# Kernel tuning notes

Measured on AMD Instinct MI355X. Metric: run time of the kernel, lower is better.

The kernel has to match this reference:

```python
import jax, jax.numpy as jnp
import numpy as np

NUM_STEPS = 20
BETA = 0.9
THR = 1.0
B, D, H, O = 8192, 784, 128, 10


def setup_inputs() -> dict:
    key = jax.random.key(0)
    k1, k2, k3, k4, k5 = jax.random.split(key, 5)
    x = jax.random.uniform(k1, (B, D), jnp.float32)  # rates in [0,1]
    lim1 = 1.0 / np.sqrt(D)
    lim2 = 1.0 / np.sqrt(H)
    fc1_w = jax.random.uniform(k2, (H, D), jnp.float32, -lim1, lim1)
    fc1_b = jax.random.uniform(k3, (H,), jnp.float32, -lim1, lim1)
    fc2_w = jax.random.uniform(k4, (O, H), jnp.float32, -lim2, lim2)
    fc2_b = jax.random.uniform(k5, (O,), jnp.float32, -lim2, lim2)
    return {"x": x, "fc1_w": fc1_w, "fc1_b": fc1_b, "fc2_w": fc2_w, "fc2_b": fc2_b}


def heaviside(u):
    return (u > 0).astype(u.dtype)


def lif_step(mem, cur):
    # snntorch Leaky, reset_mechanism='subtract':
    #   reset computed from incoming mem, then mem = beta*mem + cur - reset*thr
    reset = heaviside(mem - THR)
    mem = BETA * mem + cur - reset * THR
    spk = heaviside(mem - THR)
    return spk, mem


def reference(x, fc1_w, fc1_b, fc2_w, fc2_b):
    batch = x.shape[0]
    # spikegen.rate: per-step Bernoulli with probability x (fixed key -> deterministic)
    skey = jax.random.key(42)
    x_spike = jax.random.bernoulli(skey, x, (NUM_STEPS, batch, x.shape[1])).astype(x.dtype)

    mem1 = jnp.zeros((batch, fc1_w.shape[0]), x.dtype)
    mem2 = jnp.zeros((batch, fc2_w.shape[0]), x.dtype)

    def step(carry, x_t):
        m1, m2 = carry
        cur1 = x_t @ fc1_w.T + fc1_b          # [B,128]
        spk1, m1 = lif_step(m1, cur1)
        cur2 = spk1 @ fc2_w.T + fc2_b         # [B,10]
        spk2, m2 = lif_step(m2, cur2)
        return (m1, m2), spk2

    _, spk2_stack = jax.lax.scan(step, (mem1, mem2), x_spike)  # [T,B,10]
    return spk2_stack.sum(axis=0) / NUM_STEPS
```

## Files before the change

### kernel.cpp

```cpp
#include <hip/hip_runtime.h>
#include <cstdint>


#define T_STEPS 20
#define B_SZ   8192
#define D_SZ   784
#define H_SZ   128
#define O_SZ   10
#define CUR1_BYTES  83886080u
#define MASKS_OFF   83886080u
#define WP_OFF      84541440u
#define THR_OFF     101539840u

typedef __attribute__((ext_vector_type(8))) short short8;
typedef __attribute__((ext_vector_type(4))) float f32x4;
typedef unsigned short ushort_t;

#define ROTL_ASM(dst, src, sh)                                        \
  asm("v_alignbit_b32 %0, %1, %1, %2" : "=v"(dst) : "v"(src), "n"(32 - (sh)))

__device__ __forceinline__ void threefry_0_42(uint32_t c1,
                                              uint32_t& o0, uint32_t& o1) {
  const uint32_t ks1 = 42u;
  const uint32_t ks2 = 42u ^ 0x1BD11BDAu;
  uint32_t x0, x1, r;
  x1 = c1 + ks1;
  x0 = x1;
  ROTL_ASM(r, x1, 13); x1 = r ^ x0;
#define TF_R(rot) { x0 += x1; ROTL_ASM(r, x1, rot); x1 = r ^ x0; }
#define TF_IR(C1, K0, rot) { x1 += (C1); x0 = x0 + (K0) + x1; \
                             ROTL_ASM(r, x1, rot); x1 = r ^ x0; }
  TF_R(15) TF_R(26) TF_R(6)
  TF_IR(ks2 + 1u, ks1, 17) TF_R(29) TF_R(16) TF_R(24)
  TF_IR(2u,       ks2, 13) TF_R(15) TF_R(26) TF_R(6)
  TF_IR(ks1 + 3u, 0u,  17) TF_R(29) TF_R(16) TF_R(24)
  TF_IR(ks2 + 4u, ks1, 13) TF_R(15) TF_R(26) TF_R(6)
#undef TF_R
#undef TF_IR
  x0 += ks2; x1 += 5u;
  o0 = x0; o1 = x1;
}

__device__ __forceinline__ uint32_t rne_bf16_bits(float f) {
  uint32_t u = __float_as_uint(f);
  return (u + 0x7fffu + ((u >> 16) & 1u)) & 0xffff0000u;
}

__global__ __launch_bounds__(256) void prep(
    const float* __restrict__ w1, const float* __restrict__ x,
    ushort_t* __restrict__ wp, uint32_t* __restrict__ thresh) {
  if (blockIdx.x < 128) {
    const int h = blockIdx.x;
    for (int k = threadIdx.x; k < 800; k += 256) {
      float w = (k < D_SZ) ? w1[h * D_SZ + k] : 0.0f;
      uint32_t hb = rne_bf16_bits(w);
      float hi = __uint_as_float(hb);
      float r1 = w - hi;
      uint32_t mb = rne_bf16_bits(r1);
      float mid = __uint_as_float(mb);
      float lo = r1 - mid;
      uint32_t lb = __float_as_uint(lo);
      wp[0 * 102400 + h * 800 + k] = (ushort_t)(hb >> 16);
      wp[1 * 102400 + h * 800 + k] = (ushort_t)(mb >> 16);
      wp[2 * 102400 + h * 800 + k] = (ushort_t)(lb >> 16);
    }
  } else {
    const int gid = (blockIdx.x - 128) * 256 + threadIdx.x;
    const int b = gid / 100;
    const int y = gid - b * 100;
    const int d0 = y << 3;
    uint4 T0 = {0u, 0u, 0u, 0u}, T1 = {0u, 0u, 0u, 0u};
    if (y < 98) {
      const float* xr = x + (size_t)b * D_SZ + d0;
      float4 v0 = *(const float4*)xr;
      float4 v1 = *(const float4*)(xr + 4);
      T0.x = (uint32_t)__builtin_ceilf(v0.x * 8388608.0f) << 9;
      T0.y = (uint32_t)__builtin_ceilf(v0.y * 8388608.0f) << 9;
      T0.z = (uint32_t)__builtin_ceilf(v0.z * 8388608.0f) << 9;
      T0.w = (uint32_t)__builtin_ceilf(v0.w * 8388608.0f) << 9;
      T1.x = (uint32_t)__builtin_ceilf(v1.x * 8388608.0f) << 9;
      T1.y = (uint32_t)__builtin_ceilf(v1.y * 8388608.0f) << 9;
      T1.z = (uint32_t)__builtin_ceilf(v1.z * 8388608.0f) << 9;
      T1.w = (uint32_t)__builtin_ceilf(v1.w * 8388608.0f) << 9;
    }
    uint32_t* tp = thresh + (size_t)b * 800 + d0;
    *(uint4*)tp       = T0;
    *(uint4*)(tp + 4) = T1;
  }
}

__global__ __launch_bounds__(256) void spike_gemm(
    const uint32_t* __restrict__ thresh, const ushort_t* __restrict__ wp,
    const float* __restrict__ b1, float* __restrict__ cur1) {
  __shared__ uint32_t sM[128 * 25];
  __shared__ __align__(16) uint32_t sLUT[256][4];

  const int tid  = threadIdx.x;
  const int row0 = blockIdx.x << 7;
  const int b0   = (blockIdx.x & 63) << 7;

  {
    uint32_t v = (uint32_t)tid;
    sLUT[v][0] = ((v &   1u) ? 0x3F80u : 0u) | ((v &   2u) ? 0x3F800000u : 0u);
    sLUT[v][1] = ((v &   4u) ? 0x3F80u : 0u) | ((v &   8u) ? 0x3F800000u : 0u);
    sLUT[v][2] = ((v &  16u) ? 0x3F80u : 0u) | ((v &  32u) ? 0x3F800000u : 0u);
    sLUT[v][3] = ((v &  64u) ? 0x3F80u : 0u) | ((v & 128u) ? 0x3F800000u : 0u);
  }

  for (int idx = tid; idx < 3200; idx += 256) {
    int r = idx / 25;
    int w = idx - r * 25;
    int b = b0 + r;
    const uint32_t* tp = thresh + (size_t)b * 800 + (w << 5);
    uint32_t Ts[32];
#pragma unroll
    for (int q = 0; q < 8; ++q) {
      uint4 v = *(const uint4*)(tp + q * 4);
      Ts[q * 4 + 0] = v.x; Ts[q * 4 + 1] = v.y;
      Ts[q * 4 + 2] = v.z; Ts[q * 4 + 3] = v.w;
    }
    const uint32_t nw = (uint32_t)(row0 + r) * 784u + ((uint32_t)w << 5);
    uint32_t word = 0u;
#pragma unroll
    for (int j = 31; j >= 0; --j) {
      uint32_t o0, o1;
      threefry_0_42(nw + (uint32_t)j, o0, o1);
      uint32_t bits = o0 ^ o1;
      asm("v_cmp_lt_u32 vcc, %1, %2\n\t"
          "v_addc_co_u32 %0, vcc, %0, %0, vcc"
          : "+v"(word) : "v"(bits), "v"(Ts[j]) : "vcc");
    }
    sM[idx] = word;
  }
  __syncthreads();

  const int wave = tid >> 6, lane = tid & 63;
  const int wr0  = (wave >> 1) << 6;
  const int wc0  = (wave & 1) << 6;
  const int lm   = lane & 15, quad = lane >> 4;
  const int qsh  = quad << 3;

  f32x4 acc[4][4];
#pragma unroll
  for (int m = 0; m < 4; ++m)
#pragma unroll
    for (int nn = 0; nn < 4; ++nn) acc[m][nn] = (f32x4){0.f, 0.f, 0.f, 0.f};

  const ushort_t* wbase = wp + (size_t)(wc0 + lm) * 800 + qsh;
  const uint32_t* mrow  = &sM[(wr0 + lm) * 25];

  for (int ko = 0; ko < 25; ++ko) {
    short8 a[4];
#pragma unroll
    for (int m = 0; m < 4; ++m) {
      uint32_t word = mrow[m * 400 + ko];
      uint32_t byte = (word >> qsh) & 0xffu;
      a[m] = *(const short8*)&sLUT[byte][0];
    }
    const int kof = ko << 5;
#pragma unroll
    for (int p = 0; p < 3; ++p) {
#pragma unroll
      for (int nn = 0; nn < 4; ++nn) {
        short8 bf = *(const short8*)&wbase[p * 102400 + nn * 16 * 800 + kof];
#pragma unroll
        for (int m = 0; m < 4; ++m)
          acc[m][nn] = __builtin_amdgcn_mfma_f32_16x16x32_bf16(
              a[m], bf, acc[m][nn], 0, 0, 0);
      }
    }
  }

#pragma unroll
  for (int nn = 0; nn < 4; ++nn) {
    int col = wc0 + nn * 16 + lm;
    float bias = b1[col];
#pragma unroll
    for (int m = 0; m < 4; ++m) {
#pragma unroll
      for (int r = 0; r < 4; ++r) {
        int grow = row0 + wr0 + m * 16 + quad * 4 + r;
        cur1[(size_t)grow * H_SZ + col] = acc[m][nn][r] + bias;
      }
    }
  }
}

__global__ __launch_bounds__(256) void lif1_spikes(
    const float* __restrict__ cur1, uint32_t* __restrict__ masks) {
#pragma clang fp contract(off)
  const int g    = blockIdx.x * 256 + threadIdx.x;
  const int row  = g >> 4;
  const int s    = g & 15;
  const int lane = threadIdx.x & 63;

  float mem[8];
#pragma unroll
  for (int i = 0; i < 8; ++i) mem[i] = 0.0f;

  for (int t = 0; t < T_STEPS; ++t) {
    const float* base = cur1 + ((size_t)t * B_SZ + row) * H_SZ + s * 8;
    float4 c0 = *(const float4*)base;
    float4 c1 = *(const float4*)(base + 4);
    float cv[8] = {c0.x, c0.y, c0.z, c0.w, c1.x, c1.y, c1.z, c1.w};

    uint32_t bits8 = 0u;
#pragma unroll
    for (int q = 0; q < 8; ++q) {
      float m = mem[q];
      float reset = (m > 1.0f) ? 1.0f : 0.0f;
      m = 0.9f * m;
      m = m + cv[q];
      m = m - reset;
      mem[q] = m;
      bits8 |= (m > 1.0f) ? (1u << q) : 0u;
    }
    uint32_t part = bits8 << ((s & 3) * 8);
    part |= __shfl_xor(part, 1);
    part |= __shfl_xor(part, 2);
    uint32_t myw = __shfl(part, (lane & ~15) + 4 * (s & 3));
    if (s < 4)
      masks[((size_t)t * B_SZ + row) * 4 + s] = myw;
  }
}

__global__ __launch_bounds__(320) void lif2_seq(
    const float* __restrict__ w2, const float* __restrict__ b2,
    const uint32_t* __restrict__ masks, float* __restrict__ out) {
#pragma clang fp contract(off)
  __shared__ __align__(16) float sW2[O_SZ][H_SZ];
  const int tid = threadIdx.x;
  for (int i = tid; i < O_SZ * H_SZ; i += 320)
    sW2[i >> 7][i & 127] = w2[i];
  __syncthreads();

  const int wave = tid >> 6;
  const int lane = tid & 63;
  const int row  = ((blockIdx.x >> 1) << 6) + lane;
  const int o    = (blockIdx.x & 1) * 5 + wave;
  const float bias = b2[o];

  float mem2 = 0.0f;
  int cnt = 0;
  const uint4* mbase = (const uint4*)masks;

  for (int t = 0; t < T_STEPS; ++t) {
    uint4 m = mbase[(size_t)t * B_SZ + row];
    uint32_t mw[4] = {m.x, m.y, m.z, m.w};
    float acc = 0.0f;
#pragma unroll
    for (int w = 0; w < 4; ++w) {
#pragma unroll
      for (int hc = 0; hc < 8; ++hc) {
        float4 wv = *(const float4*)&sW2[o][w * 32 + hc * 4];
        float vv[4] = {wv.x, wv.y, wv.z, wv.w};
#pragma unroll
        for (int bb = 0; bb < 4; ++bb) {
          float val = ((mw[w] >> (hc * 4 + bb)) & 1u) ? vv[bb] : 0.0f;
          acc = acc + val;
        }
      }
    }
    float c2 = acc + bias;
    float reset = (mem2 > 1.0f) ? 1.0f : 0.0f;
    mem2 = 0.9f * mem2;
    mem2 = mem2 + c2;
    mem2 = mem2 - reset;
    cnt += (mem2 > 1.0f) ? 1 : 0;
  }
  out[row * O_SZ + o] = (float)cnt / 20.0f;
}

extern "C" void kernel_launch(void* const* d_in, const int* in_sizes, int n_in,
                              void* d_out, int out_size, void* d_ws, size_t ws_size,
                              hipStream_t stream) {
  const float* x   = (const float*)d_in[0];
  const float* w1  = (const float*)d_in[1];
  const float* b1  = (const float*)d_in[2];
  const float* w2  = (const float*)d_in[3];
  const float* b2  = (const float*)d_in[4];
  float* out  = (float*)d_out;
  float*    cur1   = (float*)d_ws;
  uint32_t* masks  = (uint32_t*)((char*)d_ws + MASKS_OFF);
  ushort_t* wp     = (ushort_t*)((char*)d_ws + WP_OFF);
  uint32_t* thresh = (uint32_t*)((char*)d_ws + THR_OFF);

  prep       <<<dim3(3328), dim3(256), 0, stream>>>(w1, x, wp, thresh);
  spike_gemm <<<dim3(1280), dim3(256), 0, stream>>>(thresh, wp, b1, cur1);
  lif1_spikes<<<dim3(512),  dim3(256), 0, stream>>>(cur1, masks);
  lif2_seq   <<<dim3(256),  dim3(320), 0, stream>>>(w2, b2, masks, out);
}
```

Measured before the change: 424.7 us.

## Fuse spike GEMM with layer-1 LIF to skip the cur1 round trip

Merges the spike-generation GEMM and the layer-1 LIF kernel into one kernel. Each block owns 16 batch rows for all 20 timesteps, processed in groups of 5, and keeps membrane state in registers. The 80 MB cur1 intermediate is never written to or read back from global memory, and one launch is removed. In exchange, only 512 blocks run with small per-wave MFMA tiles and a sync per group, so there is less parallelism and less weight reuse per block.

```diff
diff --git a/kernel.cpp b/kernel.cpp
--- a/kernel.cpp
+++ b/kernel.cpp
@@ -7,8 +7,7 @@
 #define D_SZ   784
 #define H_SZ   128
 #define O_SZ   10
-#define CUR1_BYTES  83886080u
-#define MASKS_OFF   83886080u
+#define MASKS_OFF   0u
 #define WP_OFF      84541440u
 #define THR_OFF     101539840u
 
@@ -89,15 +88,16 @@
   }
 }
 
-__global__ __launch_bounds__(256) void spike_gemm(
+__global__ __launch_bounds__(256) void spike_lif1(
     const uint32_t* __restrict__ thresh, const ushort_t* __restrict__ wp,
-    const float* __restrict__ b1, float* __restrict__ cur1) {
-  __shared__ uint32_t sM[128 * 25];
+    const float* __restrict__ b1, uint32_t* __restrict__ masks) {
+#pragma clang fp contract(off)
+  __shared__ uint32_t sM[2][5][16][25];
   __shared__ __align__(16) uint32_t sLUT[256][4];
 
-  const int tid  = threadIdx.x;
-  const int row0 = blockIdx.x << 7;
-  const int b0   = (blockIdx.x & 63) << 7;
+  const int tid    = threadIdx.x;
+  const int bid    = blockIdx.x;
+  const int b_row0 = bid << 4;
 
   {
     uint32_t v = (uint32_t)tid;
@@ -107,120 +107,119 @@
     sLUT[v][3] = ((v &  64u) ? 0x3F80u : 0u) | ((v & 128u) ? 0x3F800000u : 0u);
   }
 
-  for (int idx = tid; idx < 3200; idx += 256) {
-    int r = idx / 25;
-    int w = idx - r * 25;
-    int b = b0 + r;
-    const uint32_t* tp = thresh + (size_t)b * 800 + (w << 5);
-    uint32_t Ts[32];
-#pragma unroll
-    for (int q = 0; q < 8; ++q) {
-      uint4 v = *(const uint4*)(tp + q * 4);
-      Ts[q * 4 + 0] = v.x; Ts[q * 4 + 1] = v.y;
-      Ts[q * 4 + 2] = v.z; Ts[q * 4 + 3] = v.w;
-    }
-    const uint32_t nw = (uint32_t)(row0 + r) * 784u + ((uint32_t)w << 5);
-    uint32_t word = 0u;
-#pragma unroll
-    for (int j = 31; j >= 0; --j) {
-      uint32_t o0, o1;
-      threefry_0_42(nw + (uint32_t)j, o0, o1);
-      uint32_t bits = o0 ^ o1;
-      asm("v_cmp_lt_u32 vcc, %1, %2\n\t"
-          "v_addc_co_u32 %0, vcc, %0, %0, vcc"
-          : "+v"(word) : "v"(bits), "v"(Ts[j]) : "vcc");
-    }
-    sM[idx] = word;
-  }
-  __syncthreads();
-
   const int wave = tid >> 6, lane = tid & 63;
-  const int wr0  = (wave >> 1) << 6;
-  const int wc0  = (wave & 1) << 6;
   const int lm   = lane & 15, quad = lane >> 4;
   const int qsh  = quad << 3;
 
-  f32x4 acc[4][4];
-#pragma unroll
-  for (int m = 0; m < 4; ++m)
-#pragma unroll
-    for (int nn = 0; nn < 4; ++nn) acc[m][nn] = (f32x4){0.f, 0.f, 0.f, 0.f};
-
-  const ushort_t* wbase = wp + (size_t)(wc0 + lm) * 800 + qsh;
-  const uint32_t* mrow  = &sM[(wr0 + lm) * 25];
-
-  for (int ko = 0; ko < 25; ++ko) {
-    short8 a[4];
-#pragma unroll
-    for (int m = 0; m < 4; ++m) {
-      uint32_t word = mrow[m * 400 + ko];
-      uint32_t byte = (word >> qsh) & 0xffu;
-      a[m] = *(const short8*)&sLUT[byte][0];
-    }
-    const int kof = ko << 5;
-#pragma unroll
-    for (int p = 0; p < 3; ++p) {
-#pragma unroll
-      for (int nn = 0; nn < 4; ++nn) {
-        short8 bf = *(const short8*)&wbase[p * 102400 + nn * 16 * 800 + kof];
-#pragma unroll
-        for (int m = 0; m < 4; ++m)
-          acc[m][nn] = __builtin_amdgcn_mfma_f32_16x16x32_bf16(
-              a[m], bf, acc[m][nn], 0, 0, 0);
-      }
-    }
-  }
-
-#pragma unroll
-  for (int nn = 0; nn < 4; ++nn) {
-    int col = wc0 + nn * 16 + lm;
-    float bias = b1[col];
-#pragma unroll
-    for (int m = 0; m < 4; ++m) {
-#pragma unroll
-      for (int r = 0; r < 4; ++r) {
-        int grow = row0 + wr0 + m * 16 + quad * 4 + r;
-        cur1[(size_t)grow * H_SZ + col] = acc[m][nn][r] + bias;
-      }
-    }
-  }
-}
-
-__global__ __launch_bounds__(256) void lif1_spikes(
-    const float* __restrict__ cur1, uint32_t* __restrict__ masks) {
-#pragma clang fp contract(off)
-  const int g    = blockIdx.x * 256 + threadIdx.x;
-  const int row  = g >> 4;
-  const int s    = g & 15;
-  const int lane = threadIdx.x & 63;
-
-  float mem[8];
-#pragma unroll
-  for (int i = 0; i < 8; ++i) mem[i] = 0.0f;
-
-  for (int t = 0; t < T_STEPS; ++t) {
-    const float* base = cur1 + ((size_t)t * B_SZ + row) * H_SZ + s * 8;
-    float4 c0 = *(const float4*)base;
-    float4 c1 = *(const float4*)(base + 4);
-    float cv[8] = {c0.x, c0.y, c0.z, c0.w, c1.x, c1.y, c1.z, c1.w};
-
-    uint32_t bits8 = 0u;
-#pragma unroll
-    for (int q = 0; q < 8; ++q) {
-      float m = mem[q];
-      float reset = (m > 1.0f) ? 1.0f : 0.0f;
-      m = 0.9f * m;
-      m = m + cv[q];
-      m = m - reset;
-      mem[q] = m;
-      bits8 |= (m > 1.0f) ? (1u << q) : 0u;
-    }
-    uint32_t part = bits8 << ((s & 3) * 8);
-    part |= __shfl_xor(part, 1);
-    part |= __shfl_xor(part, 2);
-    uint32_t myw = __shfl(part, (lane & ~15) + 4 * (s & 3));
-    if (s < 4)
-      masks[((size_t)t * B_SZ + row) * 4 + s] = myw;
+  const ushort_t* wbase = wp + (size_t)(wave * 32 + lm) * 800 + qsh;
+  const float bias0 = b1[wave * 32 + lm];
+  const float bias1 = b1[wave * 32 + 16 + lm];
+
+  f32x4 mem0 = {0.f, 0.f, 0.f, 0.f};
+  f32x4 mem1 = {0.f, 0.f, 0.f, 0.f};
+
+  for (int g = 0; g < 4; ++g) {
+    const int t0  = 5 * g;
+    const int buf = g & 1;
+
+    const int base = 500 * wave;
+    for (int it = 0; it < 8; ++it) {
+      if (it < 7 || lane < 52) {
+        int widx = base + it * 64 + lane;
+        int tt  = widx / 400;
+        int rem = widx - tt * 400;
+        int r   = rem / 25;
+        int w   = rem - r * 25;
+        const uint32_t* tp = thresh + (size_t)(b_row0 + r) * 800 + (w << 5);
+        uint32_t Ts[32];
+#pragma unroll
+        for (int q = 0; q < 8; ++q) {
+          uint4 v = *(const uint4*)(tp + q * 4);
+          Ts[q * 4 + 0] = v.x; Ts[q * 4 + 1] = v.y;
+          Ts[q * 4 + 2] = v.z; Ts[q * 4 + 3] = v.w;
+        }
+        const uint32_t nw =
+            ((uint32_t)(t0 + tt) * 8192u + (uint32_t)(b_row0 + r)) * 784u +
+            ((uint32_t)w << 5);
+        uint32_t word = 0u;
+#pragma unroll
+        for (int j = 31; j >= 0; --j) {
+          uint32_t o0, o1;
+          threefry_0_42(nw + (uint32_t)j, o0, o1);
+          uint32_t bits = o0 ^ o1;
+          asm("v_cmp_lt_u32 vcc, %1, %2\n\t"
+              "v_addc_co_u32 %0, vcc, %0, %0, vcc"
+              : "+v"(word) : "v"(bits), "v"(Ts[j]) : "vcc");
+        }
+        sM[buf][tt][r][w] = word;
+      }
+    }
+    __syncthreads();
+
+    f32x4 acc[5][2];
+#pragma unroll
+    for (int tt = 0; tt < 5; ++tt) {
+      acc[tt][0] = (f32x4){0.f, 0.f, 0.f, 0.f};
+      acc[tt][1] = (f32x4){0.f, 0.f, 0.f, 0.f};
+    }
+    for (int ko = 0; ko < 25; ++ko) {
+      short8 a[5];
+#pragma unroll
+      for (int tt = 0; tt < 5; ++tt) {
+        uint32_t word = sM[buf][tt][lm][ko];
+        a[tt] = *(const short8*)&sLUT[(word >> qsh) & 0xffu][0];
+      }
+      const int kof = ko << 5;
+#pragma unroll
+      for (int p = 0; p < 3; ++p) {
+#pragma unroll
+        for (int nn = 0; nn < 2; ++nn) {
+          short8 bf = *(const short8*)&wbase[p * 102400 + nn * 12800 + kof];
+#pragma unroll
+          for (int tt = 0; tt < 5; ++tt)
+            acc[tt][nn] = __builtin_amdgcn_mfma_f32_16x16x32_bf16(
+                a[tt], bf, acc[tt][nn], 0, 0, 0);
+        }
+      }
+    }
+
+#pragma unroll
+    for (int tt = 0; tt < 5; ++tt) {
+      const int t = t0 + tt;
+      unsigned long long bk0[4], bk1[4];
+#pragma unroll
+      for (int rl = 0; rl < 4; ++rl) {
+        float cv0 = acc[tt][0][rl] + bias0;
+        float m0  = mem0[rl];
+        float r0  = (m0 > 1.0f) ? 1.0f : 0.0f;
+        m0 = 0.9f * m0;
+        m0 = m0 + cv0;
+        m0 = m0 - r0;
+        mem0[rl] = m0;
+        float cv1 = acc[tt][1][rl] + bias1;
+        float m1  = mem1[rl];
+        float r1  = (m1 > 1.0f) ? 1.0f : 0.0f;
+        m1 = 0.9f * m1;
+        m1 = m1 + cv1;
+        m1 = m1 - r1;
+        mem1[rl] = m1;
+        bk0[rl] = __ballot(m0 > 1.0f);
+        bk1[rl] = __ballot(m1 > 1.0f);
+      }
+      if (lane < 16) {
+        const int q  = lane >> 2;
+        const int rl = lane & 3;
+        unsigned long long s0 =
+            (rl & 2) ? ((rl & 1) ? bk0[3] : bk0[2])
+                     : ((rl & 1) ? bk0[1] : bk0[0]);
+        unsigned long long s1 =
+            (rl & 2) ? ((rl & 1) ? bk1[3] : bk1[2])
+                     : ((rl & 1) ? bk1[1] : bk1[0]);
+        uint32_t wd = ((uint32_t)(s0 >> (16 * q)) & 0xffffu) |
+                      (((uint32_t)(s1 >> (16 * q)) & 0xffffu) << 16);
+        masks[((size_t)t * B_SZ + b_row0 + lane) * 4 + wave] = wd;
+      }
+    }
   }
 }
 
@@ -280,13 +279,11 @@
   const float* w2  = (const float*)d_in[3];
   const float* b2  = (const float*)d_in[4];
   float* out  = (float*)d_out;
-  float*    cur1   = (float*)d_ws;
   uint32_t* masks  = (uint32_t*)((char*)d_ws + MASKS_OFF);
   ushort_t* wp     = (ushort_t*)((char*)d_ws + WP_OFF);
   uint32_t* thresh = (uint32_t*)((char*)d_ws + THR_OFF);
 
-  prep       <<<dim3(3328), dim3(256), 0, stream>>>(w1, x, wp, thresh);
-  spike_gemm <<<dim3(1280), dim3(256), 0, stream>>>(thresh, wp, b1, cur1);
-  lif1_spikes<<<dim3(512),  dim3(256), 0, stream>>>(cur1, masks);
-  lif2_seq   <<<dim3(256),  dim3(320), 0, stream>>>(w2, b2, masks, out);
-}
+  prep      <<<dim3(3328), dim3(256), 0, stream>>>(w1, x, wp, thresh);
+  spike_lif1<<<dim3(512),  dim3(256), 0, stream>>>(thresh, wp, b1, masks);
+  lif2_seq  <<<dim3(256),  dim3(320), 0, stream>>>(w2, b2, masks, out);
+}
```

Result: faster. 399.7 us (-5.9%).
